# Kernel optimization log

Measured on AMD Instinct MI355X. Metric: run time of the kernel, lower is better.

The kernel has to match this reference:

```python
import jax, jax.numpy as jnp
import numpy as np

N_NODES = 100000
N_EDGES = 1600000
N_GRAPHS = 256
D = 128
L = 3
N_OUT = 10


def setup_inputs() -> dict:
    key = jax.random.key(0)
    ks = jax.random.split(key, 6)
    x = jax.random.normal(ks[0], (N_NODES, D), dtype=jnp.float32)
    edge_index = jax.random.randint(ks[1], (2, N_EDGES), 0, N_NODES, dtype=jnp.int64)
    batch = jnp.sort(jax.random.randint(ks[2], (N_NODES,), 0, N_GRAPHS, dtype=jnp.int64))
    conv_w = jax.random.normal(ks[3], (L, D, D), dtype=jnp.float32) * (1.0 / np.sqrt(D))
    conv_b = jnp.zeros((L, D), dtype=jnp.float32)
    out_w = jax.random.normal(ks[4], (3 * D, N_OUT), dtype=jnp.float32) * (1.0 / np.sqrt(3 * D))
    out_b = jnp.zeros((N_OUT,), dtype=jnp.float32)
    return {"x": x, "edge_index": edge_index, "batch": batch,
            "conv_w": conv_w, "conv_b": conv_b, "out_w": out_w, "out_b": out_b}


def reference(x, edge_index, batch, conv_w, conv_b, out_w, out_b):
    N = x.shape[0]
    # --- add self-loops (PyG GCNConv default) ---
    loop = jnp.arange(N, dtype=edge_index.dtype)
    src = jnp.concatenate([edge_index[0], loop])  # [E+N]
    dst = jnp.concatenate([edge_index[1], loop])
    # --- symmetric normalization: deg computed on dst (col) ---
    deg = jax.ops.segment_sum(jnp.ones_like(dst, dtype=x.dtype), dst, num_segments=N)
    dinv = jnp.where(deg > 0, jax.lax.rsqrt(jnp.maximum(deg, 1.0)), 0.0)
    norm = dinv[src] * dinv[dst]  # [E+N]

    h = x
    for l in range(conv_w.shape[0]):
        h = h @ conv_w[l]                                   # [N, D] transform first
        msg = h[src] * norm[:, None]                        # gather + scale
        h = jax.ops.segment_sum(msg, dst, num_segments=N)   # scatter-add
        h = jax.nn.relu(h + conv_b[l])

    # --- global max / mean / add pooling over graphs ---
    B = N_GRAPHS
    gmax = jax.ops.segment_max(h, batch, num_segments=B)
    gsum = jax.ops.segment_sum(h, batch, num_segments=B)
    cnt = jax.ops.segment_sum(jnp.ones((N, 1), h.dtype), batch, num_segments=B)
    gmean = gsum / jnp.maximum(cnt, 1.0)
    pooled = jnp.concatenate([gmax, gmean, gsum], axis=1)   # [B, 3D]
    # dropout p=0.5 is identity in eval mode
    return pooled @ out_w + out_b
```

## Files before the change

kernel.cpp:

```cpp
#include <hip/hip_runtime.h>
#include <hip/hip_bf16.h>

#define D 128
#define NP 8

typedef __attribute__((ext_vector_type(8))) __bf16 bf16x8;
typedef __attribute__((ext_vector_type(4))) float f32x4;
typedef __attribute__((ext_vector_type(4))) short s16x4;
typedef __attribute__((ext_vector_type(8))) short s16x8;

static __device__ __forceinline__ short f2bf(float f) {
    union { float f; unsigned u; } in; in.f = f;
    unsigned u = in.u;
    u += 0x7fffu + ((u >> 16) & 1u);
    return (short)(u >> 16);
}

__global__ void k_count(const int* __restrict__ src, const int* __restrict__ dst,
                        int* __restrict__ counts, int E, int dpp, int spp) {
    int part = blockIdx.x & 7;
    int i = (blockIdx.x >> 3) * blockDim.x + threadIdx.x;
    if (i < E) {
        int d = dst[i];
        int lo = part * dpp;
        if (d >= lo && d < lo + dpp) {
            int sh = src[i] / spp; if (sh > NP - 1) sh = NP - 1;
            atomicAdd(&counts[d * NP + sh], 1);
        }
    }
}

__global__ void k_dinv(const int* __restrict__ row_ptr, float* __restrict__ dinv, int N) {
    int i = blockIdx.x * blockDim.x + threadIdx.x;
    if (i < N) {
        int deg = row_ptr[i * NP + NP] - row_ptr[i * NP];
        dinv[i] = rsqrtf((float)deg + 1.0f);
    }
}

__global__ void k_gseg(const int* __restrict__ batch, int* __restrict__ gstart,
                       int N, int B) {
    int g = blockIdx.x * blockDim.x + threadIdx.x;
    if (g > B) return;
    int lo = 0, hi = N;
    while (lo < hi) {
        int mid = (lo + hi) >> 1;
        if (batch[mid] < g) lo = mid + 1; else hi = mid;
    }
    gstart[g] = lo;
}

__global__ void k_gcnt_seg(const int* __restrict__ gstart, int* __restrict__ gcnt, int B) {
    int g = blockIdx.x * blockDim.x + threadIdx.x;
    if (g < B) gcnt[g] = gstart[g + 1] - gstart[g];
}

__global__ void k_scan1(const int* __restrict__ in, int* __restrict__ excl,
                        int* __restrict__ bsums, int len) {
    __shared__ int s[256];
    int i = blockIdx.x * 256 + threadIdx.x;
    int v = (i < len) ? in[i] : 0;
    s[threadIdx.x] = v;
    __syncthreads();
    for (int off = 1; off < 256; off <<= 1) {
        int t = (threadIdx.x >= off) ? s[threadIdx.x - off] : 0;
        __syncthreads();
        s[threadIdx.x] += t;
        __syncthreads();
    }
    if (i < len) excl[i] = s[threadIdx.x] - v;
    if (threadIdx.x == 255) bsums[blockIdx.x] = s[255];
}

__global__ void k_scan2(const int* __restrict__ bsums, int* __restrict__ boffs, int nb) {
    __shared__ int s[512];
    int t = threadIdx.x;
    int v = (t < nb) ? bsums[t] : 0;
    s[t] = v;
    __syncthreads();
    for (int off = 1; off < 512; off <<= 1) {
        int x = (t >= off) ? s[t - off] : 0;
        __syncthreads();
        s[t] += x;
        __syncthreads();
    }
    if (t < nb) boffs[t] = s[t] - v;
}

__global__ void k_scan_add(int* __restrict__ excl1, const int* __restrict__ boffs2, int len) {
    int i = blockIdx.x * 256 + threadIdx.x;
    if (i < len) excl1[i] += boffs2[blockIdx.x];
}

__global__ void k_scan3(int* __restrict__ row_ptr, int* __restrict__ cursor,
                        const int* __restrict__ boffs, int len, int E) {
    int i = blockIdx.x * 256 + threadIdx.x;
    if (i < len) {
        int r = row_ptr[i] + boffs[blockIdx.x];
        row_ptr[i] = r;
        cursor[i] = r;
    }
    if (i == 0) row_ptr[len] = E;
}

__global__ void k_fill(const int* __restrict__ src, const int* __restrict__ dst,
                       int* __restrict__ cursor, int* __restrict__ csr_src,
                       int E, int dpp, int spp) {
    int part = blockIdx.x & 7;
    int i = (blockIdx.x >> 3) * blockDim.x + threadIdx.x;
    if (i < E) {
        int d = dst[i];
        int lo = part * dpp;
        if (d >= lo && d < lo + dpp) {
            int s = src[i];
            int sh = s / spp; if (sh > NP - 1) sh = NP - 1;
            int slot = atomicAdd(&cursor[d * NP + sh], 1);
            csr_src[slot] = s;
        }
    }
}

__global__ void k_cvt_x(const float* __restrict__ x, const float* __restrict__ dinv,
                        short* __restrict__ xb, int total4) {
    int i = blockIdx.x * blockDim.x + threadIdx.x;
    if (i < total4) {
        float d = dinv[i >> 5];
        float4 v = ((const float4*)x)[i];
        s16x4 o;
        o.x = f2bf(v.x * d); o.y = f2bf(v.y * d);
        o.z = f2bf(v.z * d); o.w = f2bf(v.w * d);
        ((s16x4*)xb)[i] = o;
    }
}

__global__ void k_cvt_w(const float* __restrict__ W, short* __restrict__ Wt, int total) {
    int i = blockIdx.x * blockDim.x + threadIdx.x;
    if (i < total) {
        int l = i >> 14;
        int rem = i & 16383;
        int n = rem >> 7;
        int k = rem & 127;
        Wt[i] = f2bf(W[(l << 14) + (k << 7) + n]);
    }
}

__global__ __launch_bounds__(256) void k_aggregate(
    const short* __restrict__ hb, const int* __restrict__ row_ptr,
    const int* __restrict__ csr_src, const float* __restrict__ dinv,
    short* __restrict__ g, int N)
{
    const int wave = threadIdx.x >> 6;
    const int lane = threadIdx.x & 63;
    const int group = lane >> 4;
    const int off = (lane & 15) * 8;
    const int i = blockIdx.x * 16 + wave * 4 + group;
    if (i >= N) return;

    float acc[8];
    {
        bf16x8 v = *(const bf16x8*)(hb + (size_t)i * D + off);
        #pragma unroll
        for (int k = 0; k < 8; k++) acc[k] = (float)v[k];
    }

    const int kb = i * NP;
    int s = row_ptr[kb];
    #pragma unroll 1
    for (int p = 0; p < NP; p++) {
        int e = row_ptr[kb + p + 1];
        for (int t = s; t < e; t += 4) {
            int i0 = csr_src[t];
            int i1 = (t + 1 < e) ? csr_src[t + 1] : -1;
            int i2 = (t + 2 < e) ? csr_src[t + 2] : -1;
            int i3 = (t + 3 < e) ? csr_src[t + 3] : -1;
            bf16x8 v0 = *(const bf16x8*)(hb + (size_t)i0 * D + off);
            bf16x8 v1, v2, v3;
            if (i1 >= 0) v1 = *(const bf16x8*)(hb + (size_t)i1 * D + off);
            if (i2 >= 0) v2 = *(const bf16x8*)(hb + (size_t)i2 * D + off);
            if (i3 >= 0) v3 = *(const bf16x8*)(hb + (size_t)i3 * D + off);
            #pragma unroll
            for (int k = 0; k < 8; k++) acc[k] += (float)v0[k];
            if (i1 >= 0) {
                #pragma unroll
                for (int k = 0; k < 8; k++) acc[k] += (float)v1[k];
            }
            if (i2 >= 0) {
                #pragma unroll
                for (int k = 0; k < 8; k++) acc[k] += (float)v2[k];
            }
            if (i3 >= 0) {
                #pragma unroll
                for (int k = 0; k < 8; k++) acc[k] += (float)v3[k];
            }
        }
        s = e;
    }

    const float di = dinv[i];
    s16x8 o;
    #pragma unroll
    for (int k = 0; k < 8; k++) o[k] = f2bf(acc[k] * di);
    *(s16x8*)(g + (size_t)i * D + off) = o;
}

__global__ __launch_bounds__(256) void k_gemm(const short* __restrict__ A,
                                              const short* __restrict__ Wt,
                                              const float* __restrict__ bias,
                                              const float* __restrict__ dinv,
                                              short* __restrict__ hb_out,
                                              float* __restrict__ hrelu,
                                              int N, int mode) {
    const int wave = threadIdx.x >> 6;
    const int lane = threadIdx.x & 63;
    const int m_base = blockIdx.x * 128 + wave * 32;
    const int lr = lane & 15;
    const int lq = lane >> 4;

    bf16x8 afrag[2][4];
    #pragma unroll
    for (int rt = 0; rt < 2; rt++) {
        int m = m_base + rt * 16 + lr;
        if (m >= N) m = N - 1;
        const short* ap = A + (size_t)m * D + lq * 8;
        #pragma unroll
        for (int kt = 0; kt < 4; kt++)
            afrag[rt][kt] = *(const bf16x8*)(ap + kt * 32);
    }

    f32x4 acc[2][8];
    #pragma unroll
    for (int rt = 0; rt < 2; rt++)
        #pragma unroll
        for (int nt = 0; nt < 8; nt++) {
            f32x4 z = {0.f, 0.f, 0.f, 0.f};
            acc[rt][nt] = z;
        }

    const short* bp = Wt + lr * D + lq * 8;
    #pragma unroll
    for (int nt = 0; nt < 8; nt++) {
        #pragma unroll
        for (int kt = 0; kt < 4; kt++) {
            bf16x8 b = *(const bf16x8*)(bp + nt * 16 * D + kt * 32);
            acc[0][nt] = __builtin_amdgcn_mfma_f32_16x16x32_bf16(afrag[0][kt], b, acc[0][nt], 0, 0, 0);
            acc[1][nt] = __builtin_amdgcn_mfma_f32_16x16x32_bf16(afrag[1][kt], b, acc[1][nt], 0, 0, 0);
        }
    }

    float bcol[8];
    #pragma unroll
    for (int nt = 0; nt < 8; nt++) bcol[nt] = bias[nt * 16 + lr];

    #pragma unroll
    for (int rt = 0; rt < 2; rt++) {
        int row0 = m_base + rt * 16 + lq * 4;
        #pragma unroll
        for (int i2 = 0; i2 < 4; i2++) {
            int r = row0 + i2;
            if (r < N) {
                if (mode == 0) {
                    float dr = dinv[r];
                    #pragma unroll
                    for (int nt = 0; nt < 8; nt++) {
                        int col = nt * 16 + lr;
                        float val = fmaxf(acc[rt][nt][i2] + bcol[nt], 0.0f);
                        hb_out[(size_t)r * D + col] = f2bf(val * dr);
                    }
                } else {
                    #pragma unroll
                    for (int nt = 0; nt < 8; nt++) {
                        int col = nt * 16 + lr;
                        hrelu[(size_t)r * D + col] = fmaxf(acc[rt][nt][i2] + bcol[nt], 0.0f);
                    }
                }
            }
        }
    }
}

__global__ __launch_bounds__(256) void k_pool(const float* __restrict__ hrelu,
                                              const int* __restrict__ gstart,
                                              const int* __restrict__ gcnt,
                                              float* __restrict__ gmax,
                                              float* __restrict__ gsum) {
    int g = blockIdx.x;
    int c = threadIdx.x & 127;
    int p = threadIdx.x >> 7;
    int start = gstart[g];
    int endr = start + gcnt[g];

    float mx0 = 0.f, mx1 = 0.f, sm0 = 0.f, sm1 = 0.f;
    int r = start + p;
    for (; r + 2 < endr; r += 4) {
        float v0 = hrelu[(size_t)r * D + c];
        float v1 = hrelu[(size_t)(r + 2) * D + c];
        mx0 = fmaxf(mx0, v0); sm0 += v0;
        mx1 = fmaxf(mx1, v1); sm1 += v1;
    }
    if (r < endr) {
        float v0 = hrelu[(size_t)r * D + c];
        mx0 = fmaxf(mx0, v0); sm0 += v0;
    }
    float mx = fmaxf(mx0, mx1), sm = sm0 + sm1;

    __shared__ float smx[128], ssm[128];
    if (p == 1) { smx[c] = mx; ssm[c] = sm; }
    __syncthreads();
    if (p == 0) {
        gmax[g * D + c] = fmaxf(mx, smx[c]);
        gsum[g * D + c] = sm + ssm[c];
    }
}

__global__ void k_final(const float* __restrict__ gmax, const float* __restrict__ gsum,
                        const int* __restrict__ gcnt, const float* __restrict__ ow,
                        const float* __restrict__ ob, float* __restrict__ out) {
    int g = blockIdx.x;
    int t = threadIdx.x;
    float part[10];
    #pragma unroll
    for (int o = 0; o < 10; o++) part[o] = 0.f;
    float invc = 1.0f / fmaxf((float)gcnt[g], 1.0f);
    for (int k = t; k < 3 * D; k += 64) {
        float pk;
        if (k < D) pk = gmax[g * D + k];
        else if (k < 2 * D) pk = gsum[g * D + (k - D)] * invc;
        else pk = gsum[g * D + (k - 2 * D)];
        const float* w = ow + k * 10;
        #pragma unroll
        for (int o = 0; o < 10; o++) part[o] += pk * w[o];
    }
    #pragma unroll
    for (int off = 32; off > 0; off >>= 1)
        #pragma unroll
        for (int o = 0; o < 10; o++) part[o] += __shfl_down(part[o], off, 64);
    if (t == 0)
        #pragma unroll
        for (int o = 0; o < 10; o++) out[g * 10 + o] = part[o] + ob[o];
}

extern "C" void kernel_launch(void* const* d_in, const int* in_sizes, int n_in,
                              void* d_out, int out_size, void* d_ws, size_t ws_size,
                              hipStream_t stream) {
    const float* x     = (const float*)d_in[0];
    const int*   ei    = (const int*)d_in[1];
    const int*   batch = (const int*)d_in[2];
    const float* convw = (const float*)d_in[3];
    const float* convb = (const float*)d_in[4];
    const float* outw  = (const float*)d_in[5];
    const float* outb  = (const float*)d_in[6];
    float* out = (float*)d_out;

    const int N = in_sizes[0] / D;
    const int E = in_sizes[1] / 2;
    const int L = in_sizes[3] / (D * D);
    const int B = out_size / 10;

    const int* src = ei;
    const int* dst = ei + E;

    const int NK  = N * NP;
    const int dpp = (N + 7) / 8;
    const int spp = (N + NP - 1) / NP;

    char* p = (char*)d_ws;
    auto alloc = [&](size_t bytes) { char* r = p; p += (bytes + 255) & ~255ull; return r; };
    short* hb      = (short*)alloc((size_t)N * D * 2);
    short* gbuf    = (short*)alloc((size_t)N * D * 2);
    float* hrelu   = (float*)alloc((size_t)N * D * 4);
    short* Wt      = (short*)alloc((size_t)L * D * D * 2);
    int*   counts  = (int*)alloc((size_t)NK * 4);
    int*   row_ptr = (int*)alloc(((size_t)NK + 1) * 4);
    int*   cursor  = (int*)alloc((size_t)NK * 4);
    int*   csr_src = (int*)alloc((size_t)E * 4);
    int*   bs1     = (int*)alloc(4096 * 4);
    int*   excl1   = (int*)alloc(4096 * 4);
    int*   bs2     = (int*)alloc(64 * 4);
    int*   boffs2  = (int*)alloc(64 * 4);
    float* dinv    = (float*)alloc((size_t)N * 4);
    float* gmax    = (float*)alloc((size_t)B * D * 4);
    float* gsum    = (float*)alloc((size_t)B * D * 4);
    int*   gcnt    = (int*)alloc((size_t)B * 4);
    int*   gstart  = (int*)alloc(((size_t)B + 1) * 4);

    hipMemsetAsync(counts, 0, (size_t)NK * 4, stream);

    const int nb0 = (NK + 255) / 256;
    const int nb1 = (nb0 + 255) / 256;
    const int eblocks = 8 * ((E + 255) / 256);

    k_count<<<eblocks, 256, 0, stream>>>(src, dst, counts, E, dpp, spp);
    k_gseg<<<1, 512, 0, stream>>>(batch, gstart, N, B);
    k_gcnt_seg<<<1, 256, 0, stream>>>(gstart, gcnt, B);
    k_scan1<<<nb0, 256, 0, stream>>>(counts, row_ptr, bs1, NK);
    k_scan1<<<nb1, 256, 0, stream>>>(bs1, excl1, bs2, nb0);
    k_scan2<<<1, 512, 0, stream>>>(bs2, boffs2, nb1);
    k_scan_add<<<nb1, 256, 0, stream>>>(excl1, boffs2, nb0);
    k_scan3<<<nb0, 256, 0, stream>>>(row_ptr, cursor, excl1, NK, E);
    k_dinv<<<(N + 255) / 256, 256, 0, stream>>>(row_ptr, dinv, N);
    k_fill<<<eblocks, 256, 0, stream>>>(src, dst, cursor, csr_src, E, dpp, spp);
    k_cvt_x<<<((N * D / 4) + 255) / 256, 256, 0, stream>>>(x, dinv, hb, N * D / 4);
    k_cvt_w<<<((L * D * D) + 255) / 256, 256, 0, stream>>>(convw, Wt, L * D * D);

    const int ablocks = (N + 15) / 16;
    const int gblocks = (N + 127) / 128;
    for (int l = 0; l < L; l++) {
        k_aggregate<<<ablocks, 256, 0, stream>>>(hb, row_ptr, csr_src, dinv, gbuf, N);
        k_gemm<<<gblocks, 256, 0, stream>>>(gbuf, Wt + l * D * D, convb + (size_t)l * D,
                                            dinv, hb, hrelu, N, (l == L - 1) ? 1 : 0);
    }
    k_pool<<<B, 256, 0, stream>>>(hrelu, gstart, gcnt, gmax, gsum);
    k_final<<<B, 64, 0, stream>>>(gmax, gsum, gcnt, outw, outb, out);
}
```

Before: 566.9 us.

## Build CSR via destination bucketing and per-block shared-memory counting sort

Replaces the global atomic count, multi-level scan and atomic fill passes with a two-level counting sort. Edges are first bucketed by destination range into a staging buffer (reusing the hrelu buffer), then each block sorts its bucket in shared memory, writes row_ptr and csr_src, and computes dinv. This cuts the number of kernel launches and replaces scattered global atomics with LDS atomics. In exchange it relies on a fixed per-bucket capacity (CAP) and packs the key and source index into 17-bit fields, so skewed inputs or larger node counts would silently drop or corrupt edges.

```diff
diff --git a/kernel.cpp b/kernel.cpp
--- a/kernel.cpp
+++ b/kernel.cpp
@@ -3,6 +3,9 @@
 
 #define D 128
 #define NP 8
+#define KB 512
+#define CAP 8192
+#define KPB_MAX 1600
 
 typedef __attribute__((ext_vector_type(8))) __bf16 bf16x8;
 typedef __attribute__((ext_vector_type(4))) float f32x4;
@@ -16,25 +19,95 @@
     return (short)(u >> 16);
 }
 
-__global__ void k_count(const int* __restrict__ src, const int* __restrict__ dst,
-                        int* __restrict__ counts, int E, int dpp, int spp) {
-    int part = blockIdx.x & 7;
-    int i = (blockIdx.x >> 3) * blockDim.x + threadIdx.x;
-    if (i < E) {
-        int d = dst[i];
-        int lo = part * dpp;
-        if (d >= lo && d < lo + dpp) {
-            int sh = src[i] / spp; if (sh > NP - 1) sh = NP - 1;
-            atomicAdd(&counts[d * NP + sh], 1);
-        }
-    }
-}
-
-__global__ void k_dinv(const int* __restrict__ row_ptr, float* __restrict__ dinv, int N) {
-    int i = blockIdx.x * blockDim.x + threadIdx.x;
-    if (i < N) {
-        int deg = row_ptr[i * NP + NP] - row_ptr[i * NP];
-        dinv[i] = rsqrtf((float)deg + 1.0f);
+__global__ void k_bucket(const int* __restrict__ src, const int* __restrict__ dst,
+                         int* __restrict__ bcnt, int* __restrict__ staging,
+                         int E, int dpb, int spp) {
+    int i = blockIdx.x * 256 + threadIdx.x;
+    if (i >= E) return;
+    int d = dst[i], s = src[i];
+    int b = d / dpb;
+    int dl = d - b * dpb;
+    int sh = s / spp; if (sh > NP - 1) sh = NP - 1;
+    int key = dl * NP + sh;
+    int slot = atomicAdd(&bcnt[b], 1);
+    if (slot < CAP) staging[(size_t)b * CAP + slot] = (key << 17) | s;
+}
+
+__global__ void k_bscan(const int* __restrict__ bcnt, int* __restrict__ bbase,
+                        int* __restrict__ row_ptr, int E, int nkeys) {
+    __shared__ int sm[KB];
+    int t = threadIdx.x;
+    int v = bcnt[t];
+    sm[t] = v;
+    __syncthreads();
+    for (int off = 1; off < KB; off <<= 1) {
+        int x = (t >= off) ? sm[t - off] : 0;
+        __syncthreads();
+        sm[t] += x;
+        __syncthreads();
+    }
+    bbase[t] = sm[t] - v;
+    if (t == 0) row_ptr[nkeys] = E;
+}
+
+__global__ __launch_bounds__(256) void k_build(
+    const int* __restrict__ staging, const int* __restrict__ bcnt,
+    const int* __restrict__ bbase, int* __restrict__ row_ptr,
+    int* __restrict__ csr_src, float* __restrict__ dinv, int N, int dpb)
+{
+    const int b = blockIdx.x;
+    const int tid = threadIdx.x;
+    const int kpb = dpb * NP;
+    int nb = bcnt[b]; if (nb > CAP) nb = CAP;
+    const int base = bbase[b];
+    __shared__ int cnt[KPB_MAX];
+    __shared__ int chunkbuf[256];
+    __shared__ int carry;
+
+    for (int k = tid; k < kpb; k += 256) cnt[k] = 0;
+    if (tid == 0) carry = 0;
+    __syncthreads();
+
+    const int* sb = staging + (size_t)b * CAP;
+    for (int t = tid; t < nb; t += 256)
+        atomicAdd(&cnt[sb[t] >> 17], 1);
+    __syncthreads();
+
+    const int nchunk = (kpb + 255) / 256;
+    for (int c = 0; c < nchunk; c++) {
+        int idx = c * 256 + tid;
+        int v = (idx < kpb) ? cnt[idx] : 0;
+        chunkbuf[tid] = v;
+        __syncthreads();
+        for (int off = 1; off < 256; off <<= 1) {
+            int x = (tid >= off) ? chunkbuf[tid - off] : 0;
+            __syncthreads();
+            chunkbuf[tid] += x;
+            __syncthreads();
+        }
+        int excl = chunkbuf[tid] - v + carry;
+        if (idx < kpb) cnt[idx] = excl;
+        __syncthreads();
+        if (tid == 255) carry += chunkbuf[255];
+        __syncthreads();
+    }
+
+    for (int k = tid; k < kpb; k += 256)
+        row_ptr[(size_t)b * kpb + k] = base + cnt[k];
+    for (int dl = tid; dl < dpb; dl += 256) {
+        int d = b * dpb + dl;
+        if (d < N) {
+            int hi = (dl == dpb - 1) ? nb : cnt[(dl + 1) * NP];
+            int deg = hi - cnt[dl * NP];
+            dinv[d] = rsqrtf((float)deg + 1.0f);
+        }
+    }
+    __syncthreads();
+
+    for (int t = tid; t < nb; t += 256) {
+        int w = sb[t];
+        int slot = base + atomicAdd(&cnt[w >> 17], 1);
+        csr_src[slot] = w & 0x1FFFF;
     }
 }
 
@@ -53,71 +126,6 @@
 __global__ void k_gcnt_seg(const int* __restrict__ gstart, int* __restrict__ gcnt, int B) {
     int g = blockIdx.x * blockDim.x + threadIdx.x;
     if (g < B) gcnt[g] = gstart[g + 1] - gstart[g];
-}
-
-__global__ void k_scan1(const int* __restrict__ in, int* __restrict__ excl,
-                        int* __restrict__ bsums, int len) {
-    __shared__ int s[256];
-    int i = blockIdx.x * 256 + threadIdx.x;
-    int v = (i < len) ? in[i] : 0;
-    s[threadIdx.x] = v;
-    __syncthreads();
-    for (int off = 1; off < 256; off <<= 1) {
-        int t = (threadIdx.x >= off) ? s[threadIdx.x - off] : 0;
-        __syncthreads();
-        s[threadIdx.x] += t;
-        __syncthreads();
-    }
-    if (i < len) excl[i] = s[threadIdx.x] - v;
-    if (threadIdx.x == 255) bsums[blockIdx.x] = s[255];
-}
-
-__global__ void k_scan2(const int* __restrict__ bsums, int* __restrict__ boffs, int nb) {
-    __shared__ int s[512];
-    int t = threadIdx.x;
-    int v = (t < nb) ? bsums[t] : 0;
-    s[t] = v;
-    __syncthreads();
-    for (int off = 1; off < 512; off <<= 1) {
-        int x = (t >= off) ? s[t - off] : 0;
-        __syncthreads();
-        s[t] += x;
-        __syncthreads();
-    }
-    if (t < nb) boffs[t] = s[t] - v;
-}
-
-__global__ void k_scan_add(int* __restrict__ excl1, const int* __restrict__ boffs2, int len) {
-    int i = blockIdx.x * 256 + threadIdx.x;
-    if (i < len) excl1[i] += boffs2[blockIdx.x];
-}
-
-__global__ void k_scan3(int* __restrict__ row_ptr, int* __restrict__ cursor,
-                        const int* __restrict__ boffs, int len, int E) {
-    int i = blockIdx.x * 256 + threadIdx.x;
-    if (i < len) {
-        int r = row_ptr[i] + boffs[blockIdx.x];
-        row_ptr[i] = r;
-        cursor[i] = r;
-    }
-    if (i == 0) row_ptr[len] = E;
-}
-
-__global__ void k_fill(const int* __restrict__ src, const int* __restrict__ dst,
-                       int* __restrict__ cursor, int* __restrict__ csr_src,
-                       int E, int dpp, int spp) {
-    int part = blockIdx.x & 7;
-    int i = (blockIdx.x >> 3) * blockDim.x + threadIdx.x;
-    if (i < E) {
-        int d = dst[i];
-        int lo = part * dpp;
-        if (d >= lo && d < lo + dpp) {
-            int s = src[i];
-            int sh = s / spp; if (sh > NP - 1) sh = NP - 1;
-            int slot = atomicAdd(&cursor[d * NP + sh], 1);
-            csr_src[slot] = s;
-        }
-    }
 }
 
 __global__ void k_cvt_x(const float* __restrict__ x, const float* __restrict__ dinv,
@@ -359,9 +367,10 @@
     const int* src = ei;
     const int* dst = ei + E;
 
-    const int NK  = N * NP;
-    const int dpp = (N + 7) / 8;
-    const int spp = (N + NP - 1) / NP;
+    const int dpb   = (N + KB - 1) / KB;
+    const int kpb   = dpb * NP;
+    const int nkeys = KB * kpb;
+    const int spp   = (N + NP - 1) / NP;
 
     char* p = (char*)d_ws;
     auto alloc = [&](size_t bytes) { char* r = p; p += (bytes + 255) & ~255ull; return r; };
@@ -369,36 +378,25 @@
     short* gbuf    = (short*)alloc((size_t)N * D * 2);
     float* hrelu   = (float*)alloc((size_t)N * D * 4);
     short* Wt      = (short*)alloc((size_t)L * D * D * 2);
-    int*   counts  = (int*)alloc((size_t)NK * 4);
-    int*   row_ptr = (int*)alloc(((size_t)NK + 1) * 4);
-    int*   cursor  = (int*)alloc((size_t)NK * 4);
+    int*   row_ptr = (int*)alloc(((size_t)nkeys + 1) * 4);
     int*   csr_src = (int*)alloc((size_t)E * 4);
-    int*   bs1     = (int*)alloc(4096 * 4);
-    int*   excl1   = (int*)alloc(4096 * 4);
-    int*   bs2     = (int*)alloc(64 * 4);
-    int*   boffs2  = (int*)alloc(64 * 4);
+    int*   bcnt    = (int*)alloc((size_t)KB * 4);
+    int*   bbase   = (int*)alloc((size_t)KB * 4);
     float* dinv    = (float*)alloc((size_t)N * 4);
     float* gmax    = (float*)alloc((size_t)B * D * 4);
     float* gsum    = (float*)alloc((size_t)B * D * 4);
     int*   gcnt    = (int*)alloc((size_t)B * 4);
     int*   gstart  = (int*)alloc(((size_t)B + 1) * 4);
 
-    hipMemsetAsync(counts, 0, (size_t)NK * 4, stream);
-
-    const int nb0 = (NK + 255) / 256;
-    const int nb1 = (nb0 + 255) / 256;
-    const int eblocks = 8 * ((E + 255) / 256);
-
-    k_count<<<eblocks, 256, 0, stream>>>(src, dst, counts, E, dpp, spp);
+    int* staging = (int*)hrelu;
+
+    hipMemsetAsync(bcnt, 0, (size_t)KB * 4, stream);
+
+    k_bucket<<<(E + 255) / 256, 256, 0, stream>>>(src, dst, bcnt, staging, E, dpb, spp);
     k_gseg<<<1, 512, 0, stream>>>(batch, gstart, N, B);
     k_gcnt_seg<<<1, 256, 0, stream>>>(gstart, gcnt, B);
-    k_scan1<<<nb0, 256, 0, stream>>>(counts, row_ptr, bs1, NK);
-    k_scan1<<<nb1, 256, 0, stream>>>(bs1, excl1, bs2, nb0);
-    k_scan2<<<1, 512, 0, stream>>>(bs2, boffs2, nb1);
-    k_scan_add<<<nb1, 256, 0, stream>>>(excl1, boffs2, nb0);
-    k_scan3<<<nb0, 256, 0, stream>>>(row_ptr, cursor, excl1, NK, E);
-    k_dinv<<<(N + 255) / 256, 256, 0, stream>>>(row_ptr, dinv, N);
-    k_fill<<<eblocks, 256, 0, stream>>>(src, dst, cursor, csr_src, E, dpp, spp);
+    k_bscan<<<1, KB, 0, stream>>>(bcnt, bbase, row_ptr, E, nkeys);
+    k_build<<<KB, 256, 0, stream>>>(staging, bcnt, bbase, row_ptr, csr_src, dinv, N, dpb);
     k_cvt_x<<<((N * D / 4) + 255) / 256, 256, 0, stream>>>(x, dinv, hb, N * D / 4);
     k_cvt_w<<<((L * D * D) + 255) / 256, 256, 0, stream>>>(convw, Wt, L * D * D);
 
```

Measured after the change: 918.8 us. 62.1% more time.
